# Kernel tuning notes

Hardware: AMD Instinct MI355X
Metric: run time of the kernel (lower is better)

The kernel has to match this reference:

```python
import jax, jax.numpy as jnp
import numpy as np

C = 16          # n_tasks (channels) = num_tasks - 1
NUM_TASKS = 17  # IndexKernel size
RANK = 3        # IndexKernel rank (hard-coded in source)
JITTER = 1e-4
N_MC = 10
N_CLASSES = 10

def _rbf(x1, x2, ls):
    d = (x1[:, None] - x2[None, :]) / ls
    return jnp.exp(-0.5 * d * d)

def _gp_posterior(x, i_tr, y, xs, i_te, c, ls, noise, Btask):
    # Exact GP posterior with Hadamard multitask kernel k(x,x')*B[i,i'].
    T = x.shape[0]
    Kxx = _rbf(x, x, ls) * Btask[i_tr][:, i_tr] + (noise * noise + JITTER) * jnp.eye(T, dtype=x.dtype)
    Ksx = _rbf(xs, x, ls) * Btask[i_te][:, i_tr]
    Kss = _rbf(xs, xs, ls) * Btask[i_te][:, i_te]
    L = jnp.linalg.cholesky(Kxx)
    alpha = jax.scipy.linalg.cho_solve((L, True), y - c)
    mean = c + Ksx @ alpha
    V = jax.scipy.linalg.solve_triangular(L, Ksx.T, lower=True)  # [T, Ts]
    cov = Kss - V.T @ V
    return mean, cov

def _channel_reshape(Z_raw, test_idx):
    # Vectorized version of the triple-loop ragged scatter.
    # Z_raw: [S, B, Ts]; test_idx: [B, Ts] int -> Z: [S, B, max_len, C]
    S, Bb, Ts = Z_raw.shape
    max_len = Ts // C
    onehot = jax.nn.one_hot(test_idx, C, dtype=jnp.int32)                       # [B, Ts, C]
    before = jnp.cumsum(onehot, axis=1) - onehot                                # same-channel count before elem
    pos = jnp.take_along_axis(before, test_idx[..., None], axis=-1)[..., 0]     # [B, Ts]
    b_idx = jnp.broadcast_to(jnp.arange(Bb)[:, None], (Bb, Ts))
    Z = jnp.zeros((S, Bb, max_len, C), Z_raw.dtype)
    return Z.at[:, b_idx, pos, test_idx].set(Z_raw)

def setup_inputs() -> dict:
    key = jax.random.key(0)
    ks = jax.random.split(key, 8)
    B, T, Ts = 32, 1024, 1024
    inputs = jax.random.uniform(ks[0], (B, T, 1), jnp.float32) * 10.0
    indices = jax.random.randint(ks[1], (B, T, 1), 0, C)
    values = jax.random.normal(ks[2], (B, T), jnp.float32)
    test_inputs = jax.random.uniform(ks[3], (B, Ts, 1), jnp.float32) * 10.0
    test_indices = (jnp.arange(Ts, dtype=jnp.int32)[None, :, None] % C) * jnp.ones((B, 1, 1), jnp.int32)
    eps = jax.random.normal(ks[4], (N_MC, B, Ts), jnp.float32)
    mean_const = jnp.zeros((), jnp.float32)
    lengthscale = jnp.ones((), jnp.float32)
    noise = 0.3 * jnp.ones((), jnp.float32)
    W_task = jax.random.normal(ks[5], (NUM_TASKS, RANK), jnp.float32) * 0.3
    v_task = jax.random.uniform(ks[6], (NUM_TASKS,), jnp.float32)
    W_clf = jax.random.normal(ks[7], (C, N_CLASSES), jnp.float32) * 0.1
    b_clf = jnp.zeros((N_CLASSES,), jnp.float32)
    return dict(inputs=inputs, values=values, test_inputs=test_inputs, eps=eps,
                mean_const=mean_const, lengthscale=lengthscale, noise=noise,
                W_task=W_task, v_task=v_task, W_clf=W_clf, b_clf=b_clf,
                indices=indices, test_indices=test_indices)

def reference(inputs, values, test_inputs, eps, mean_const, lengthscale, noise,
              W_task, v_task, W_clf, b_clf, indices, test_indices):
    Btask = W_task @ W_task.T + jnp.diag(jax.nn.softplus(v_task))  # IndexKernel: B = W W^T + diag(v)
    x, xs = inputs[..., 0], test_inputs[..., 0]
    i_tr, i_te = indices[..., 0], test_indices[..., 0]
    mean, cov = jax.vmap(_gp_posterior, in_axes=(0, 0, 0, 0, 0, None, None, None, None))(
        x, i_tr, values, xs, i_te, mean_const, lengthscale, noise, Btask)
    Ts = xs.shape[1]
    Lstar = jnp.linalg.cholesky(cov + JITTER * jnp.eye(Ts, dtype=cov.dtype))
    samples = mean[None] + jnp.einsum('bij,sbj->sbi', Lstar, eps)   # rsample: [S, B, Ts]
    Z = _channel_reshape(samples, i_te)                              # [S, B, max_len, C]
    S, Bb, ml, _ = Z.shape
    Zc = Z.reshape(S * Bb, ml, C)                                    # monte_carlo collapse (flatten(0,1))
    feat = Zc.mean(axis=1)                                           # clf: mean pool + linear
    return feat @ W_clf + b_clf
```

## Files before the change

kernel.cpp:

```cpp
#include <hip/hip_runtime.h>
#include <math.h>

#define TT 1024
#define CH 16
#define SMC 10
#define NCLS 10
#define JIT 1e-4f

__device__ __forceinline__ void tri_map(int tau, int& ti, int& tj) {
    int i = 0, r = tau;
    while (r >= i + 1) { r -= i + 1; i++; }
    ti = i; tj = r;
}

__global__ __launch_bounds__(256) void k_btask(const float* __restrict__ W,
                                               const float* __restrict__ v,
                                               float* __restrict__ Bt) {
    int t = threadIdx.x;
    for (int e = t; e < 17 * 17; e += 256) {
        int i = e / 17, j = e % 17;
        float s = 0.f;
        for (int r = 0; r < 3; r++) s += W[i * 3 + r] * W[j * 3 + r];
        if (i == j) s += log1pf(expf(v[i]));
        Bt[e] = s;
    }
}

__global__ __launch_bounds__(256) void k_build_kxx(const float* __restrict__ x,
                                                   const int* __restrict__ itr,
                                                   const float* __restrict__ lsp,
                                                   const float* __restrict__ noisep,
                                                   const float* __restrict__ Bt,
                                                   float* __restrict__ A, int b0) {
    int bi = blockIdx.x, bj = blockIdx.y, bz = blockIdx.z;
    if (bj > bi) return;
    int b = b0 + bz;
    __shared__ float sxi[128], sxj[128], Btl[289];
    __shared__ int sii[128], sij[128];
    int t = threadIdx.x;
    if (t < 128) { sxi[t] = x[b * TT + bi * 128 + t]; sii[t] = itr[b * TT + bi * 128 + t]; }
    else { int u = t - 128; sxj[u] = x[b * TT + bj * 128 + u]; sij[u] = itr[b * TT + bj * 128 + u]; }
    for (int e = t; e < 289; e += 256) Btl[e] = Bt[e];
    __syncthreads();
    float invls = 1.0f / lsp[0];
    float n2 = noisep[0] * noisep[0] + JIT;
    float* Ab = A + (size_t)bz * TT * TT;
    for (int l = 0; l < 64; l++) {
        int e = l * 256 + t;
        int r = e >> 7, c = e & 127;
        float d = (sxi[r] - sxj[c]) * invls;
        float kv = expf(-0.5f * d * d) * Btl[sii[r] * 17 + sij[c]];
        int gi = bi * 128 + r, gj = bj * 128 + c;
        if (gi == gj) kv += n2;
        Ab[(size_t)gi * TT + gj] = kv;
    }
}

__global__ __launch_bounds__(256) void k_build_g(const float* __restrict__ xs,
                                                 const float* __restrict__ x,
                                                 const int* __restrict__ ite,
                                                 const int* __restrict__ itr,
                                                 const float* __restrict__ lsp,
                                                 const float* __restrict__ Bt,
                                                 float* __restrict__ G, int b0) {
    int bj = blockIdx.x, bi = blockIdx.y, bz = blockIdx.z;
    int b = b0 + bz;
    __shared__ float sxr[128], sxc[128], Btl[289];
    __shared__ int sir[128], sic[128];
    int t = threadIdx.x;
    if (t < 128) { sxr[t] = x[b * TT + bj * 128 + t]; sir[t] = itr[b * TT + bj * 128 + t]; }
    else { int u = t - 128; sxc[u] = xs[b * TT + bi * 128 + u]; sic[u] = ite[b * TT + bi * 128 + u]; }
    for (int e = t; e < 289; e += 256) Btl[e] = Bt[e];
    __syncthreads();
    float invls = 1.0f / lsp[0];
    float* Gb = G + (size_t)bz * TT * TT;
    for (int l = 0; l < 64; l++) {
        int e = l * 256 + t;
        int r = e >> 7, c = e & 127;
        float d = (sxc[c] - sxr[r]) * invls;
        float kv = expf(-0.5f * d * d) * Btl[sic[c] * 17 + sir[r]];
        Gb[(size_t)(bj * 128 + r) * TT + bi * 128 + c] = kv;
    }
}

__global__ __launch_bounds__(256) void k_zinit(const float* __restrict__ values,
                                               const float* __restrict__ mc,
                                               float* __restrict__ zb, int b0) {
    int bz = blockIdx.x, t = threadIdx.x;
    float c0 = mc[0];
    for (int i = t; i < TT; i += 256) zb[bz * TT + i] = values[(size_t)(b0 + bz) * TT + i] - c0;
}

__global__ __launch_bounds__(256) void k_factor0(const float* __restrict__ A,
                                                 float* __restrict__ Dfac) {
    int bz = blockIdx.x;
    const float* Ab = A + (size_t)bz * TT * TT;
    __shared__ float Ld[64][65];
    __shared__ float invl[64];
    int t = threadIdx.x;
    for (int l = 0; l < 16; l++) {
        int e = l * 256 + t; int r = e >> 6, c = e & 63;
        Ld[r][c] = Ab[(size_t)r * TT + c];
    }
    __syncthreads();
    for (int j = 0; j < 64; j++) {
        if (t == j) { float d = sqrtf(Ld[j][j]); Ld[j][j] = d; invl[j] = 1.0f / d; }
        __syncthreads();
        float lij = 0.f;
        if (t < 64 && t > j) { lij = Ld[t][j] * invl[j]; Ld[t][j] = lij; }
        __syncthreads();
        if (t < 64 && t > j) {
#pragma unroll 4
            for (int p = j + 1; p <= t; p++) Ld[t][p] -= lij * Ld[p][j];
        }
    }
    __syncthreads();
    float* Df = Dfac + (size_t)bz * 16 * 4096;
    for (int l = 0; l < 16; l++) {
        int e = l * 256 + t; int r = e >> 6, c = e & 63;
        Df[r * 64 + c] = Ld[r][c];
    }
}

__global__ __launch_bounds__(256) void k_solveA(float* __restrict__ A,
                                                float* __restrict__ G,
                                                float* __restrict__ zb,
                                                const float* __restrict__ Dfac,
                                                int k, int m, int withG) {
    int bx = blockIdx.x, bz = blockIdx.y;
    float* Ab = A + (size_t)bz * TT * TT;
    float* Gb = G + (size_t)bz * TT * TT;
    int kb = k * 64;
    __shared__ float Ld[64][65];
    __shared__ float WK[64][129];
    __shared__ float invl[64];
    __shared__ float zs[64];
    int t = threadIdx.x;
    const float* Df = Dfac + ((size_t)bz * 16 + k) * 4096;
    for (int l = 0; l < 16; l++) {
        int e = l * 256 + t; int r = e >> 6, c = e & 63;
        Ld[r][c] = Df[r * 64 + c];
    }
    int jtype, r0 = 0, c0 = 0;
    if (bx < m) {
        jtype = 1; r0 = kb + 64 * (bx + 1);
        for (int l = 0; l < 16; l++) {
            int e = l * 256 + t; int r = e >> 6, c = e & 63;
            WK[r][c] = Ab[(size_t)(r0 + r) * TT + kb + c];
        }
    } else if (withG && bx < m + 8) {
        jtype = 2; c0 = (bx - m) * 128;
        for (int l = 0; l < 32; l++) {
            int e = l * 256 + t; int r = e >> 7, c = e & 127;
            WK[r][c] = Gb[(size_t)(kb + r) * TT + c0 + c];
        }
    } else {
        jtype = 3;
        if (t < 64) zs[t] = zb[bz * TT + kb + t];
    }
    __syncthreads();
    if (t < 64) invl[t] = 1.0f / Ld[t][t];
    __syncthreads();
    if (jtype == 1) {
        if (t < 64) {
            for (int j = 0; j < 64; j++) {
                float xv = WK[t][j] * invl[j];
                WK[t][j] = xv;
#pragma unroll 4
                for (int p = j + 1; p < 64; p++) WK[t][p] -= Ld[p][j] * xv;
            }
        }
        __syncthreads();
        for (int l = 0; l < 16; l++) {
            int e = l * 256 + t; int r = e >> 6, c = e & 63;
            Ab[(size_t)(r0 + r) * TT + kb + c] = WK[r][c];
        }
    } else if (jtype == 2) {
        if (t < 128) {
            for (int j = 0; j < 64; j++) {
                float xv = WK[j][t] * invl[j];
                WK[j][t] = xv;
#pragma unroll 4
                for (int p = j + 1; p < 64; p++) WK[p][t] -= Ld[p][j] * xv;
            }
        }
        __syncthreads();
        for (int l = 0; l < 32; l++) {
            int e = l * 256 + t; int r = e >> 7, c = e & 127;
            Gb[(size_t)(kb + r) * TT + c0 + c] = WK[r][c];
        }
    } else {
        if (t == 0) {
            for (int j = 0; j < 64; j++) {
                float zv = zs[j] * invl[j];
                zs[j] = zv;
#pragma unroll 4
                for (int p = j + 1; p < 64; p++) zs[p] -= Ld[p][j] * zv;
            }
        }
        __syncthreads();
        if (t < 64) zb[bz * TT + kb + t] = zs[t];
    }
}

__global__ __launch_bounds__(256) void k_diagfix64(float* __restrict__ A,
                                                   const float* __restrict__ Dfac) {
    int k = blockIdx.x, bz = blockIdx.y;
    int kb = k * 64;
    float* Ab = A + (size_t)bz * TT * TT;
    const float* Df = Dfac + ((size_t)bz * 16 + k) * 4096;
    int t = threadIdx.x;
    for (int l = 0; l < 16; l++) {
        int e = l * 256 + t; int r = e >> 6, c = e & 63;
        if (c <= r) Ab[(size_t)(kb + r) * TT + kb + c] = Df[r * 64 + c];
    }
}

__global__ __launch_bounds__(256) void k_stepB64(float* __restrict__ A,
                                                 float* __restrict__ G,
                                                 float* __restrict__ zb,
                                                 float* __restrict__ Dfac,
                                                 int k, int m, int bc, int withG) {
    int lin = blockIdx.x;
    int slot = lin & 7, q = lin >> 3;
    int beta = ((slot - 4 * (q & 1)) & 7) + (blockIdx.y << 3);
    if (beta >= bc) return;
    float* Ab = A + (size_t)beta * TT * TT;
    float* Gb = G + (size_t)beta * TT * TT;
    int kb = k * 64;
    int nt = (64 * m + 127) / 128;
    int TL = nt * (nt + 1) / 2;
    int gz = withG ? 9 * nt : 0;
    __shared__ __align__(16) float sm[8448];
    float (*At)[132] = reinterpret_cast<float (*)[132]>(sm);
    float (*Bs)[132] = reinterpret_cast<float (*)[132]>(sm + 4224);
    float (*FLd)[65] = reinterpret_cast<float (*)[65]>(sm);
    float (*FPn)[65] = reinterpret_cast<float (*)[65]>(sm + 4160);
    __shared__ float zk[64];
    __shared__ float finv[64];
    int t = threadIdx.x, tx = t & 15, ty = t >> 4;
    if (q < TL) {
        int ti, tj; tri_map(q, ti, tj);
        int base = kb + 64;
        int r0 = base + ti * 128, c0 = base + tj * 128;
        int rvi = TT - r0; if (rvi > 128) rvi = 128;
        int rvj = TT - c0; if (rvj > 128) rvj = 128;
        float acc[8][8] = {};
        for (int s = 0; s < 2; s++) {
            int k0 = kb + s * 32;
            __syncthreads();
            for (int l = 0; l < 4; l++) {
                int f = l * 256 + t;
                int r = f >> 3, c4 = (f & 7) * 4;
                float4 va = make_float4(0.f, 0.f, 0.f, 0.f), vb = make_float4(0.f, 0.f, 0.f, 0.f);
                if (r < rvi) va = *reinterpret_cast<const float4*>(&Ab[(size_t)(r0 + r) * TT + k0 + c4]);
                if (r < rvj) vb = *reinterpret_cast<const float4*>(&Ab[(size_t)(c0 + r) * TT + k0 + c4]);
                At[c4 + 0][r] = va.x; At[c4 + 1][r] = va.y; At[c4 + 2][r] = va.z; At[c4 + 3][r] = va.w;
                Bs[c4 + 0][r] = vb.x; Bs[c4 + 1][r] = vb.y; Bs[c4 + 2][r] = vb.z; Bs[c4 + 3][r] = vb.w;
            }
            __syncthreads();
#pragma unroll 4
            for (int p = 0; p < 32; p++) {
                float4 a0 = *reinterpret_cast<const float4*>(&At[p][ty * 8]);
                float4 a1 = *reinterpret_cast<const float4*>(&At[p][ty * 8 + 4]);
                float4 b0 = *reinterpret_cast<const float4*>(&Bs[p][tx * 4]);
                float4 b1 = *reinterpret_cast<const float4*>(&Bs[p][tx * 4 + 64]);
                float aa[8] = {a0.x, a0.y, a0.z, a0.w, a1.x, a1.y, a1.z, a1.w};
                float bl[4] = {b0.x, b0.y, b0.z, b0.w};
                float bh[4] = {b1.x, b1.y, b1.z, b1.w};
                for (int i = 0; i < 8; i++) {
                    for (int j = 0; j < 4; j++) acc[i][j] += aa[i] * bl[j];
                    for (int j = 0; j < 4; j++) acc[i][j + 4] += aa[i] * bh[j];
                }
            }
        }
        if (tx * 4 >= rvj) return;
        for (int i = 0; i < 8; i++) {
            int rr = ty * 8 + i;
            if (rr >= rvi) break;
            if (!(q == 0 && rr < 64)) {
                float* cp0 = &Ab[(size_t)(r0 + rr) * TT + c0 + tx * 4];
                float4 cv0 = *reinterpret_cast<float4*>(cp0);
                cv0.x -= acc[i][0]; cv0.y -= acc[i][1]; cv0.z -= acc[i][2]; cv0.w -= acc[i][3];
                *reinterpret_cast<float4*>(cp0) = cv0;
            }
            if (rvj > 64) {
                float* cp1 = &Ab[(size_t)(r0 + rr) * TT + c0 + 64 + tx * 4];
                float4 cv1 = *reinterpret_cast<float4*>(cp1);
                cv1.x -= acc[i][4]; cv1.y -= acc[i][5]; cv1.z -= acc[i][6]; cv1.w -= acc[i][7];
                *reinterpret_cast<float4*>(cp1) = cv1;
            }
        }
        return;
    }
    if (q < TL + gz) {
        int e = q - TL;
        int ti = e / 9, sub = e % 9;
        int r0 = kb + 64 + ti * 128;
        int rvi = TT - r0; if (rvi > 128) rvi = 128;
        if (sub < 8) {
            int c0 = sub * 128;
            float acc[8][8] = {};
            for (int s = 0; s < 2; s++) {
                int k0 = kb + s * 32;
                __syncthreads();
                for (int l = 0; l < 4; l++) {
                    int f = l * 256 + t;
                    int r = f >> 3, c4 = (f & 7) * 4;
                    float4 va = make_float4(0.f, 0.f, 0.f, 0.f);
                    if (r < rvi) va = *reinterpret_cast<const float4*>(&Ab[(size_t)(r0 + r) * TT + k0 + c4]);
                    At[c4 + 0][r] = va.x; At[c4 + 1][r] = va.y; At[c4 + 2][r] = va.z; At[c4 + 3][r] = va.w;
                    int kr = f >> 5, cc4 = (f & 31) * 4;
                    float4 vb = *reinterpret_cast<const float4*>(&Gb[(size_t)(k0 + kr) * TT + c0 + cc4]);
                    *reinterpret_cast<float4*>(&Bs[kr][cc4]) = vb;
                }
                __syncthreads();
#pragma unroll 4
                for (int p = 0; p < 32; p++) {
                    float4 a0 = *reinterpret_cast<const float4*>(&At[p][ty * 8]);
                    float4 a1 = *reinterpret_cast<const float4*>(&At[p][ty * 8 + 4]);
                    float4 b0 = *reinterpret_cast<const float4*>(&Bs[p][tx * 4]);
                    float4 b1 = *reinterpret_cast<const float4*>(&Bs[p][tx * 4 + 64]);
                    float aa[8] = {a0.x, a0.y, a0.z, a0.w, a1.x, a1.y, a1.z, a1.w};
                    float bl[4] = {b0.x, b0.y, b0.z, b0.w};
                    float bh[4] = {b1.x, b1.y, b1.z, b1.w};
                    for (int i = 0; i < 8; i++) {
                        for (int j = 0; j < 4; j++) acc[i][j] += aa[i] * bl[j];
                        for (int j = 0; j < 4; j++) acc[i][j + 4] += aa[i] * bh[j];
                    }
                }
            }
            for (int i = 0; i < 8; i++) {
                int rr = ty * 8 + i;
                if (rr >= rvi) break;
                float* cp0 = &Gb[(size_t)(r0 + rr) * TT + c0 + tx * 4];
                float4 cv0 = *reinterpret_cast<float4*>(cp0);
                cv0.x -= acc[i][0]; cv0.y -= acc[i][1]; cv0.z -= acc[i][2]; cv0.w -= acc[i][3];
                *reinterpret_cast<float4*>(cp0) = cv0;
                float* cp1 = cp0 + 64;
                float4 cv1 = *reinterpret_cast<float4*>(cp1);
                cv1.x -= acc[i][4]; cv1.y -= acc[i][5]; cv1.z -= acc[i][6]; cv1.w -= acc[i][7];
                *reinterpret_cast<float4*>(cp1) = cv1;
            }
        } else {
            if (t < 64) zk[t] = zb[beta * TT + kb + t];
            float accz = 0.f;
            for (int s = 0; s < 2; s++) {
                int k0 = kb + s * 32;
                __syncthreads();
                for (int l = 0; l < 4; l++) {
                    int f = l * 256 + t;
                    int r = f >> 3, c4 = (f & 7) * 4;
                    float4 va = make_float4(0.f, 0.f, 0.f, 0.f);
                    if (r < rvi) va = *reinterpret_cast<const float4*>(&Ab[(size_t)(r0 + r) * TT + k0 + c4]);
                    At[c4 + 0][r] = va.x; At[c4 + 1][r] = va.y; At[c4 + 2][r] = va.z; At[c4 + 3][r] = va.w;
                }
                __syncthreads();
                if (t < 128) {
                    for (int qq = 0; qq < 32; qq++) accz += At[qq][t] * zk[s * 32 + qq];
                }
            }
            if (t < rvi) zb[beta * TT + r0 + t] -= accz;
        }
        return;
    }
    {
        int kb2 = kb + 64;
        for (int l = 0; l < 16; l++) {
            int e = l * 256 + t; int r = e >> 6, c = e & 63;
            FLd[r][c] = Ab[(size_t)(kb2 + r) * TT + kb2 + c];
            FPn[r][c] = Ab[(size_t)(kb2 + r) * TT + kb + c];
        }
        __syncthreads();
        {
            float acc[4][4] = {};
            for (int p = 0; p < 64; p++) {
                float a0 = FPn[ty * 4 + 0][p], a1 = FPn[ty * 4 + 1][p];
                float a2 = FPn[ty * 4 + 2][p], a3 = FPn[ty * 4 + 3][p];
                float b0 = FPn[tx * 4 + 0][p], b1 = FPn[tx * 4 + 1][p];
                float b2 = FPn[tx * 4 + 2][p], b3 = FPn[tx * 4 + 3][p];
                acc[0][0] += a0 * b0; acc[0][1] += a0 * b1; acc[0][2] += a0 * b2; acc[0][3] += a0 * b3;
                acc[1][0] += a1 * b0; acc[1][1] += a1 * b1; acc[1][2] += a1 * b2; acc[1][3] += a1 * b3;
                acc[2][0] += a2 * b0; acc[2][1] += a2 * b1; acc[2][2] += a2 * b2; acc[2][3] += a2 * b3;
                acc[3][0] += a3 * b0; acc[3][1] += a3 * b1; acc[3][2] += a3 * b2; acc[3][3] += a3 * b3;
            }
            for (int i = 0; i < 4; i++)
                for (int j = 0; j < 4; j++)
                    FLd[ty * 4 + i][tx * 4 + j] -= acc[i][j];
        }
        __syncthreads();
        for (int j = 0; j < 64; j++) {
            if (t == j) { float d = sqrtf(FLd[j][j]); FLd[j][j] = d; finv[j] = 1.0f / d; }
            __syncthreads();
            float lij = 0.f;
            if (t < 64 && t > j) { lij = FLd[t][j] * finv[j]; FLd[t][j] = lij; }
            __syncthreads();
            if (t < 64 && t > j) {
#pragma unroll 4
                for (int p = j + 1; p <= t; p++) FLd[t][p] -= lij * FLd[p][j];
            }
        }
        __syncthreads();
        float* DfO = Dfac + ((size_t)beta * 16 + (k + 1)) * 4096;
        for (int l = 0; l < 16; l++) {
            int e = l * 256 + t; int r = e >> 6, c = e & 63;
            DfO[r * 64 + c] = FLd[r][c];
        }
    }
}

__global__ __launch_bounds__(256) void k_cov64(const float* __restrict__ G,
                                               const float* __restrict__ xs,
                                               const int* __restrict__ ite,
                                               const float* __restrict__ lsp,
                                               const float* __restrict__ Bt,
                                               float* __restrict__ A,
                                               const float* __restrict__ zb,
                                               const float* __restrict__ mc,
                                               float* __restrict__ meanb,
                                               int b0, int bc) {
    int lin = blockIdx.x;
    int slot = lin & 7, tau = lin >> 3;
    int beta = ((slot - 4 * (tau & 1)) & 7) + (blockIdx.y << 3);
    if (beta >= bc) return;
    int ti, tj; tri_map(tau, ti, tj);
    int b = b0 + beta;
    const float* Gb = G + (size_t)beta * TT * TT;
    float* Ab = A + (size_t)beta * TT * TT;
    int i0 = ti * 64, j0 = tj * 64;
    __shared__ __align__(16) float Va[32][68];
    __shared__ __align__(16) float Vb[32][68];
    __shared__ float sxi[64], sxj[64], Btl[289], zs[32];
    __shared__ int sei[64], sej[64];
    int t = threadIdx.x, tx = t & 15, ty = t >> 4;
    if (t < 64) { sxi[t] = xs[b * TT + i0 + t]; sei[t] = ite[b * TT + i0 + t]; }
    else if (t < 128) { int u = t - 64; sxj[u] = xs[b * TT + j0 + u]; sej[u] = ite[b * TT + j0 + u]; }
    for (int e = t; e < 289; e += 256) Btl[e] = Bt[e];
    bool diag = (ti == tj);
    float acc[4][4] = {};
    float macc[4] = {0.f, 0.f, 0.f, 0.f};
    for (int k0 = 0; k0 < TT; k0 += 32) {
        __syncthreads();
        for (int l = 0; l < 2; l++) {
            int f = l * 256 + t;
            int kr = f >> 4, cc4 = (f & 15) * 4;
            *reinterpret_cast<float4*>(&Va[kr][cc4]) =
                *reinterpret_cast<const float4*>(&Gb[(size_t)(k0 + kr) * TT + i0 + cc4]);
            *reinterpret_cast<float4*>(&Vb[kr][cc4]) =
                *reinterpret_cast<const float4*>(&Gb[(size_t)(k0 + kr) * TT + j0 + cc4]);
        }
        if (diag && t < 32) zs[t] = zb[beta * TT + k0 + t];
        __syncthreads();
#pragma unroll 4
        for (int p = 0; p < 32; p++) {
            float4 av = *reinterpret_cast<const float4*>(&Va[p][ty * 4]);
            float4 bv = *reinterpret_cast<const float4*>(&Vb[p][tx * 4]);
            float aa[4] = {av.x, av.y, av.z, av.w};
            float bb[4] = {bv.x, bv.y, bv.z, bv.w};
            for (int i = 0; i < 4; i++)
                for (int j = 0; j < 4; j++) acc[i][j] += aa[i] * bb[j];
        }
        if (diag && ty == 0) {
#pragma unroll 4
            for (int p = 0; p < 32; p++) {
                float zv = zs[p];
                float4 av = *reinterpret_cast<const float4*>(&Va[p][tx * 4]);
                macc[0] += av.x * zv; macc[1] += av.y * zv;
                macc[2] += av.z * zv; macc[3] += av.w * zv;
            }
        }
    }
    float invls = 1.0f / lsp[0];
    for (int i = 0; i < 4; i++) {
        int ri = ty * 4 + i; int gi = i0 + ri;
        float xi = sxi[ri]; int ci = sei[ri] * 17;
        float vo[4];
        for (int j = 0; j < 4; j++) {
            int rj = tx * 4 + j; int gj = j0 + rj;
            float d = (xi - sxj[rj]) * invls;
            float v = expf(-0.5f * d * d) * Btl[ci + sej[rj]] - acc[i][j];
            if (gi == gj) v += JIT;
            vo[j] = v;
        }
        *reinterpret_cast<float4*>(&Ab[(size_t)gi * TT + j0 + tx * 4]) =
            make_float4(vo[0], vo[1], vo[2], vo[3]);
    }
    if (diag && ty == 0) {
        float c0 = mc[0];
        for (int j = 0; j < 4; j++)
            meanb[(size_t)b * TT + i0 + tx * 4 + j] = c0 + macc[j];
    }
}

__global__ __launch_bounds__(256) void k_P(const float* __restrict__ A,
                                           const int* __restrict__ ite,
                                           float* __restrict__ P, int b0) {
    int bz = blockIdx.y; int b = b0 + bz;
    const float* Ab = A + (size_t)bz * TT * TT;
    __shared__ int chl[TT];
    __shared__ float accl[CH * 256];
    int t = threadIdx.x;
    for (int i = t; i < TT; i += 256) chl[i] = ite[b * TT + i];
    for (int c = 0; c < CH; c++) accl[c * 256 + t] = 0.f;
    __syncthreads();
    int j0 = blockIdx.x * 256;
    int j = j0 + t;
    for (int i = j0; i < TT; i++) {
        float v = Ab[(size_t)i * TT + j];
        if (i >= j) accl[chl[i] * 256 + t] += v;
    }
    for (int c = 0; c < CH; c++) P[((size_t)b * CH + c) * TT + j] = accl[c * 256 + t];
}

__global__ __launch_bounds__(64) void k_msum(const float* __restrict__ meanb,
                                             const int* __restrict__ ite,
                                             float* __restrict__ msum, int b0) {
    int bz = blockIdx.x; int b = b0 + bz;
    __shared__ float pacc[CH][65];
    int t = threadIdx.x;
    for (int c = 0; c < CH; c++) pacc[c][t] = 0.f;
    __syncthreads();
    for (int i = t; i < TT; i += 64) pacc[ite[b * TT + i]][t] += meanb[b * TT + i];
    __syncthreads();
    if (t < CH) {
        float s = 0.f;
        for (int u = 0; u < 64; u++) s += pacc[t][u];
        msum[b * CH + t] = s;
    }
}

__global__ __launch_bounds__(256) void k_featout(const float* __restrict__ P,
                                                 const float* __restrict__ msum,
                                                 const float* __restrict__ eps,
                                                 const float* __restrict__ Wc,
                                                 const float* __restrict__ bc_,
                                                 float* __restrict__ out, int b0, int Btot) {
    int s = blockIdx.x; int b = b0 + blockIdx.y;
    __shared__ float el[TT];
    __shared__ float part[256];
    __shared__ float featl[CH];
    int t = threadIdx.x;
    for (int i = t; i < TT; i += 256) el[i] = eps[((size_t)s * Btot + b) * TT + i];
    __syncthreads();
    int c = t >> 4, seg = t & 15;
    float acc = 0.f;
    const float* Pr = &P[((size_t)b * CH + c) * TT + seg * 64];
    for (int j = 0; j < 64; j++) acc += Pr[j] * el[seg * 64 + j];
    part[t] = acc;
    __syncthreads();
    if (t < CH) {
        float s2 = msum[b * CH + t];
        for (int g = 0; g < 16; g++) s2 += part[t * 16 + g];
        featl[t] = s2 * (1.0f / 64.0f);
    }
    __syncthreads();
    if (t < NCLS) {
        float o = bc_[t];
        for (int c2 = 0; c2 < CH; c2++) o += featl[c2] * Wc[c2 * NCLS + t];
        out[((size_t)s * Btot + b) * NCLS + t] = o;
    }
}

extern "C" void kernel_launch(void* const* d_in, const int* in_sizes, int n_in,
                              void* d_out, int out_size, void* d_ws, size_t ws_size,
                              hipStream_t stream) {
    const float* inputs       = (const float*)d_in[0];
    const float* values       = (const float*)d_in[1];
    const float* test_inputs  = (const float*)d_in[2];
    const float* eps          = (const float*)d_in[3];
    const float* mc           = (const float*)d_in[4];
    const float* ls           = (const float*)d_in[5];
    const float* noise        = (const float*)d_in[6];
    const float* W_task       = (const float*)d_in[7];
    const float* v_task       = (const float*)d_in[8];
    const float* W_clf        = (const float*)d_in[9];
    const float* b_clf        = (const float*)d_in[10];
    const int*   indices      = (const int*)d_in[11];
    const int*   test_indices = (const int*)d_in[12];
    float* out = (float*)d_out;

    int Btot = in_sizes[1] / TT;

    float* ws = (float*)d_ws;
    size_t off = 0;
    float* Bt    = ws + off; off += 512;
    float* zbuf  = ws + off; off += (size_t)Btot * TT;
    float* meanb = ws + off; off += (size_t)Btot * TT;
    float* Pb    = ws + off; off += (size_t)Btot * CH * TT;
    float* msum  = ws + off; off += (size_t)Btot * CH;
    off = (off + 63) & ~(size_t)63;

    size_t avail = (ws_size / 4 > off) ? (ws_size / 4 - off) : 0;
    size_t per = 2 * (size_t)TT * TT + 16 * 4096;
    int chunk = (int)(avail / per);
    if (chunk < 1) chunk = 1;
    if (chunk > Btot) chunk = Btot;
    float* bigA = ws + off;
    float* bigG = bigA + (size_t)chunk * TT * TT;
    float* Dfac = bigG + (size_t)chunk * TT * TT;

    k_btask<<<1, 256, 0, stream>>>(W_task, v_task, Bt);

    for (int b0 = 0; b0 < Btot; b0 += chunk) {
        int bcc = chunk; if (b0 + bcc > Btot) bcc = Btot - b0;
        int by = (bcc + 7) / 8;

        k_build_kxx<<<dim3(8, 8, bcc), 256, 0, stream>>>(inputs, indices, ls, noise, Bt, bigA, b0);
        k_build_g<<<dim3(8, 8, bcc), 256, 0, stream>>>(test_inputs, inputs, test_indices, indices, ls, Bt, bigG, b0);
        k_zinit<<<bcc, 256, 0, stream>>>(values, mc, zbuf, b0);
        k_factor0<<<bcc, 256, 0, stream>>>(bigA, Dfac);
        for (int k = 0; k < 16; k++) {
            int m = 15 - k;
            k_solveA<<<dim3(m + 9, bcc), 256, 0, stream>>>(bigA, bigG, zbuf, Dfac, k, m, 1);
            if (m > 0) {
                int nt = (64 * m + 127) / 128;
                int nq = nt * (nt + 1) / 2 + 9 * nt + 1;
                k_stepB64<<<dim3(nq * 8, by), 256, 0, stream>>>(bigA, bigG, zbuf, Dfac, k, m, bcc, 1);
            }
        }
        k_cov64<<<dim3(136 * 8, by), 256, 0, stream>>>(bigG, test_inputs, test_indices, ls, Bt,
                                                       bigA, zbuf, mc, meanb, b0, bcc);
        k_factor0<<<bcc, 256, 0, stream>>>(bigA, Dfac);
        for (int k = 0; k < 16; k++) {
            int m = 15 - k;
            if (m > 0) {
                k_solveA<<<dim3(m, bcc), 256, 0, stream>>>(bigA, bigA, zbuf, Dfac, k, m, 0);
                int nt = (64 * m + 127) / 128;
                int nq = nt * (nt + 1) / 2 + 1;
                k_stepB64<<<dim3(nq * 8, by), 256, 0, stream>>>(bigA, bigA, zbuf, Dfac, k, m, bcc, 0);
            }
        }
        k_diagfix64<<<dim3(16, bcc), 256, 0, stream>>>(bigA, Dfac);
        k_P<<<dim3(4, bcc), 256, 0, stream>>>(bigA, test_indices, Pb, b0);
        k_msum<<<bcc, 64, 0, stream>>>(meanb, test_indices, msum, b0);
        k_featout<<<dim3(SMC, bcc), 256, 0, stream>>>(Pb, msum, eps, W_clf, b_clf, out, b0, Btot);
    }
}
```

Baseline: 9.590 ms.

## Fuse small tail kernels and parallelize P reduction over row segments

Folds the z-init into k_build_g and the mean-sum into k_featout, and drops the separate diagfix kernel by having k_P read diagonal blocks straight from Dfac. k_P is split over 16 row segments per batch, with atomicAdd accumulation into a P buffer that k_cov64 zeroes. The goal is fewer launches and more parallelism in the tail stage. In exchange it adds atomics, makes float summation order nondeterministic, and adds a per-element channel test in featout.

```diff
diff --git a/kernel.cpp b/kernel.cpp
--- a/kernel.cpp
+++ b/kernel.cpp
@@ -62,7 +62,10 @@
                                                  const int* __restrict__ itr,
                                                  const float* __restrict__ lsp,
                                                  const float* __restrict__ Bt,
-                                                 float* __restrict__ G, int b0) {
+                                                 float* __restrict__ G,
+                                                 const float* __restrict__ values,
+                                                 const float* __restrict__ mc,
+                                                 float* __restrict__ zb, int b0) {
     int bj = blockIdx.x, bi = blockIdx.y, bz = blockIdx.z;
     int b = b0 + bz;
     __shared__ float sxr[128], sxc[128], Btl[289];
@@ -81,14 +84,10 @@
         float kv = expf(-0.5f * d * d) * Btl[sic[c] * 17 + sir[r]];
         Gb[(size_t)(bj * 128 + r) * TT + bi * 128 + c] = kv;
     }
-}
-
-__global__ __launch_bounds__(256) void k_zinit(const float* __restrict__ values,
-                                               const float* __restrict__ mc,
-                                               float* __restrict__ zb, int b0) {
-    int bz = blockIdx.x, t = threadIdx.x;
-    float c0 = mc[0];
-    for (int i = t; i < TT; i += 256) zb[bz * TT + i] = values[(size_t)(b0 + bz) * TT + i] - c0;
+    if (bi == 0 && bj == 0) {
+        float c0 = mc[0];
+        for (int i = t; i < TT; i += 256) zb[bz * TT + i] = values[(size_t)b * TT + i] - c0;
+    }
 }
 
 __global__ __launch_bounds__(256) void k_factor0(const float* __restrict__ A,
@@ -200,19 +199,6 @@
         }
         __syncthreads();
         if (t < 64) zb[bz * TT + kb + t] = zs[t];
-    }
-}
-
-__global__ __launch_bounds__(256) void k_diagfix64(float* __restrict__ A,
-                                                   const float* __restrict__ Dfac) {
-    int k = blockIdx.x, bz = blockIdx.y;
-    int kb = k * 64;
-    float* Ab = A + (size_t)bz * TT * TT;
-    const float* Df = Dfac + ((size_t)bz * 16 + k) * 4096;
-    int t = threadIdx.x;
-    for (int l = 0; l < 16; l++) {
-        int e = l * 256 + t; int r = e >> 6, c = e & 63;
-        if (c <= r) Ab[(size_t)(kb + r) * TT + kb + c] = Df[r * 64 + c];
     }
 }
 
@@ -418,6 +404,7 @@
                                                const float* __restrict__ zb,
                                                const float* __restrict__ mc,
                                                float* __restrict__ meanb,
+                                               float* __restrict__ P,
                                                int b0, int bc) {
     int lin = blockIdx.x;
     int slot = lin & 7, tau = lin >> 3;
@@ -485,71 +472,81 @@
         *reinterpret_cast<float4*>(&Ab[(size_t)gi * TT + j0 + tx * 4]) =
             make_float4(vo[0], vo[1], vo[2], vo[3]);
     }
-    if (diag && ty == 0) {
-        float c0 = mc[0];
-        for (int j = 0; j < 4; j++)
-            meanb[(size_t)b * TT + i0 + tx * 4 + j] = c0 + macc[j];
+    if (diag) {
+        if (ty == 0) {
+            float c0 = mc[0];
+            for (int j = 0; j < 4; j++)
+                meanb[(size_t)b * TT + i0 + tx * 4 + j] = c0 + macc[j];
+        }
+        if (t < 64) {
+            for (int c = 0; c < CH; c++)
+                P[((size_t)b * CH + c) * TT + i0 + t] = 0.f;
+        }
     }
 }
 
 __global__ __launch_bounds__(256) void k_P(const float* __restrict__ A,
+                                           const float* __restrict__ Dfac,
                                            const int* __restrict__ ite,
                                            float* __restrict__ P, int b0) {
-    int bz = blockIdx.y; int b = b0 + bz;
+    int jb = blockIdx.x, iseg = blockIdx.y, bz = blockIdx.z;
+    int j = jb * 256 + threadIdx.x;
+    if (iseg * 64 + 63 < jb * 256) return;
+    int b = b0 + bz;
     const float* Ab = A + (size_t)bz * TT * TT;
-    __shared__ int chl[TT];
+    const float* Df = Dfac + ((size_t)bz * 16 + iseg) * 4096;
+    __shared__ int chl[64];
     __shared__ float accl[CH * 256];
     int t = threadIdx.x;
-    for (int i = t; i < TT; i += 256) chl[i] = ite[b * TT + i];
+    if (t < 64) chl[t] = ite[b * TT + iseg * 64 + t];
     for (int c = 0; c < CH; c++) accl[c * 256 + t] = 0.f;
     __syncthreads();
-    int j0 = blockIdx.x * 256;
-    int j = j0 + t;
-    for (int i = j0; i < TT; i++) {
-        float v = Ab[(size_t)i * TT + j];
-        if (i >= j) accl[chl[i] * 256 + t] += v;
-    }
-    for (int c = 0; c < CH; c++) P[((size_t)b * CH + c) * TT + j] = accl[c * 256 + t];
-}
-
-__global__ __launch_bounds__(64) void k_msum(const float* __restrict__ meanb,
-                                             const int* __restrict__ ite,
-                                             float* __restrict__ msum, int b0) {
-    int bz = blockIdx.x; int b = b0 + bz;
-    __shared__ float pacc[CH][65];
-    int t = threadIdx.x;
-    for (int c = 0; c < CH; c++) pacc[c][t] = 0.f;
-    __syncthreads();
-    for (int i = t; i < TT; i += 64) pacc[ite[b * TT + i]][t] += meanb[b * TT + i];
-    __syncthreads();
-    if (t < CH) {
-        float s = 0.f;
-        for (int u = 0; u < 64; u++) s += pacc[t][u];
-        msum[b * CH + t] = s;
+    int jblk = j >> 6;
+    for (int l = 0; l < 64; l++) {
+        int i = iseg * 64 + l;
+        if (i >= j) {
+            float v = (jblk == iseg) ? Df[l * 64 + (j & 63)] : Ab[(size_t)i * TT + j];
+            accl[chl[l] * 256 + t] += v;
+        }
+    }
+    for (int c = 0; c < CH; c++) {
+        float s = accl[c * 256 + t];
+        if (s != 0.f) atomicAdd(&P[((size_t)b * CH + c) * TT + j], s);
     }
 }
 
 __global__ __launch_bounds__(256) void k_featout(const float* __restrict__ P,
-                                                 const float* __restrict__ msum,
+                                                 const float* __restrict__ meanb,
+                                                 const int* __restrict__ ite,
                                                  const float* __restrict__ eps,
                                                  const float* __restrict__ Wc,
                                                  const float* __restrict__ bc_,
                                                  float* __restrict__ out, int b0, int Btot) {
     int s = blockIdx.x; int b = b0 + blockIdx.y;
     __shared__ float el[TT];
+    __shared__ float ml[TT];
+    __shared__ int cl[TT];
     __shared__ float part[256];
     __shared__ float featl[CH];
     int t = threadIdx.x;
-    for (int i = t; i < TT; i += 256) el[i] = eps[((size_t)s * Btot + b) * TT + i];
+    for (int i = t; i < TT; i += 256) {
+        el[i] = eps[((size_t)s * Btot + b) * TT + i];
+        ml[i] = meanb[(size_t)b * TT + i];
+        cl[i] = ite[(size_t)b * TT + i];
+    }
     __syncthreads();
     int c = t >> 4, seg = t & 15;
     float acc = 0.f;
     const float* Pr = &P[((size_t)b * CH + c) * TT + seg * 64];
-    for (int j = 0; j < 64; j++) acc += Pr[j] * el[seg * 64 + j];
+    for (int j = 0; j < 64; j++) {
+        int idx = seg * 64 + j;
+        acc += Pr[j] * el[idx];
+        if (cl[idx] == c) acc += ml[idx];
+    }
     part[t] = acc;
     __syncthreads();
     if (t < CH) {
-        float s2 = msum[b * CH + t];
+        float s2 = 0.f;
         for (int g = 0; g < 16; g++) s2 += part[t * 16 + g];
         featl[t] = s2 * (1.0f / 64.0f);
     }
@@ -587,7 +584,6 @@
     float* zbuf  = ws + off; off += (size_t)Btot * TT;
     float* meanb = ws + off; off += (size_t)Btot * TT;
     float* Pb    = ws + off; off += (size_t)Btot * CH * TT;
-    float* msum  = ws + off; off += (size_t)Btot * CH;
     off = (off + 63) & ~(size_t)63;
 
     size_t avail = (ws_size / 4 > off) ? (ws_size / 4 - off) : 0;
@@ -606,8 +602,8 @@
         int by = (bcc + 7) / 8;
 
         k_build_kxx<<<dim3(8, 8, bcc), 256, 0, stream>>>(inputs, indices, ls, noise, Bt, bigA, b0);
-        k_build_g<<<dim3(8, 8, bcc), 256, 0, stream>>>(test_inputs, inputs, test_indices, indices, ls, Bt, bigG, b0);
-        k_zinit<<<bcc, 256, 0, stream>>>(values, mc, zbuf, b0);
+        k_build_g<<<dim3(8, 8, bcc), 256, 0, stream>>>(test_inputs, inputs, test_indices, indices,
+                                                       ls, Bt, bigG, values, mc, zbuf, b0);
         k_factor0<<<bcc, 256, 0, stream>>>(bigA, Dfac);
         for (int k = 0; k < 16; k++) {
             int m = 15 - k;
@@ -619,7 +615,7 @@
             }
         }
         k_cov64<<<dim3(136 * 8, by), 256, 0, stream>>>(bigG, test_inputs, test_indices, ls, Bt,
-                                                       bigA, zbuf, mc, meanb, b0, bcc);
+                                                       bigA, zbuf, mc, meanb, Pb, b0, bcc);
         k_factor0<<<bcc, 256, 0, stream>>>(bigA, Dfac);
         for (int k = 0; k < 16; k++) {
             int m = 15 - k;
@@ -630,9 +626,7 @@
                 k_stepB64<<<dim3(nq * 8, by), 256, 0, stream>>>(bigA, bigA, zbuf, Dfac, k, m, bcc, 0);
             }
         }
-        k_diagfix64<<<dim3(16, bcc), 256, 0, stream>>>(bigA, Dfac);
-        k_P<<<dim3(4, bcc), 256, 0, stream>>>(bigA, test_indices, Pb, b0);
-        k_msum<<<bcc, 64, 0, stream>>>(meanb, test_indices, msum, b0);
-        k_featout<<<dim3(SMC, bcc), 256, 0, stream>>>(Pb, msum, eps, W_clf, b_clf, out, b0, Btot);
-    }
-}
+        k_P<<<dim3(4, 16, bcc), 256, 0, stream>>>(bigA, Dfac, test_indices, Pb, b0);
+        k_featout<<<dim3(SMC, bcc), 256, 0, stream>>>(Pb, meanb, test_indices, eps, W_clf, b_clf, out, b0, Btot);
+    }
+}
```

Result: faster. 9.070 ms (-5.4%).
